# Optimization experiments

Measured on AMD Instinct MI355X. Metric: run time of the kernel, lower is better.

## Reference

```python
import jax, jax.numpy as jnp
import numpy as np

B, T, C, H, L, V = 64, 256, 256, 8, 6, 96
EPS = 1e-5


def _layernorm(x, w, b):
    m = x.mean(-1, keepdims=True)
    v = x.var(-1, keepdims=True)
    return (x - m) / jnp.sqrt(v + EPS) * w + b


def setup_inputs() -> dict:
    key = jax.random.key(0)
    ks = jax.random.split(key, 16)
    s = 0.05
    n = lambda k, sh: jax.random.normal(k, sh, jnp.float32) * s
    return {
        'idx': jax.random.randint(ks[0], (B, T), 0, V),
        'target': jax.random.randint(ks[1], (B, T), 0, V),
        'tok_emb': n(ks[2], (V, C)),
        'pos_emb': n(ks[3], (T, C)),
        'Wq': n(ks[4], (L, C, C)),
        'Wk': n(ks[5], (L, C, C)),
        'Wv': n(ks[6], (L, C, C)),
        'Wo': n(ks[7], (L, C, C)),
        'bo': jnp.zeros((L, C), jnp.float32),
        'W1': n(ks[8], (L, C, C)),
        'b1': jnp.zeros((L, C), jnp.float32),
        'W2': n(ks[9], (L, C, C)),
        'b2': jnp.zeros((L, C), jnp.float32),
        'ln1_w': jnp.ones((L, C), jnp.float32),
        'ln1_b': jnp.zeros((L, C), jnp.float32),
        'ln2_w': jnp.ones((L, C), jnp.float32),
        'ln2_b': jnp.zeros((L, C), jnp.float32),
        'lnf_w': jnp.ones((C,), jnp.float32),
        'lnf_b': jnp.zeros((C,), jnp.float32),
        'Wlm': n(ks[10], (C, V)),
        'blm': jnp.zeros((V,), jnp.float32),
    }


def _forward(idx, target, tok_emb, pos_emb, Wq, Wk, Wv, Wo, bo, W1, b1, W2, b2,
             ln1_w, ln1_b, ln2_w, ln2_b, lnf_w, lnf_b, Wlm, blm):
    Bc, Tc = idx.shape
    hs = C // H
    scale = C ** (-0.5)  # NOTE: original scales by n_embed**-0.5, not head_size**-0.5
    x = tok_emb[idx] + pos_emb[:Tc]              # [B,T,C]
    causal = jnp.tril(jnp.ones((Tc, Tc), bool))  # [T,T]
    for l in range(L):
        q = (x @ Wq[l]).reshape(Bc, Tc, H, hs)
        k = (x @ Wk[l]).reshape(Bc, Tc, H, hs)
        v = (x @ Wv[l]).reshape(Bc, Tc, H, hs)
        w = jnp.einsum('bqhd,bkhd->bhqk', q, k) * scale
        w = jnp.where(causal, w, -jnp.inf)
        w = jax.nn.softmax(w, axis=-1)
        att = jnp.einsum('bhqk,bkhd->bqhd', w, v).reshape(Bc, Tc, C)
        x = _layernorm(x + att @ Wo[l] + bo[l], ln1_w[l], ln1_b[l])  # post-residual LN
        h = jax.nn.relu(x @ W1[l] + b1[l]) @ W2[l] + b2[l]
        x = _layernorm(x + h, ln2_w[l], ln2_b[l])
    x = _layernorm(x, lnf_w, lnf_b)
    logits = (x @ Wlm + blm).reshape(Bc * Tc, V)
    logp = jax.nn.log_softmax(logits, axis=-1)
    nll = -jnp.take_along_axis(logp, target.reshape(-1, 1), axis=1)
    loss = nll.mean()
    return logits, loss


def reference(idx, target, tok_emb, pos_emb, Wq, Wk, Wv, Wo, bo, W1, b1, W2, b2,
              ln1_w, ln1_b, ln2_w, ln2_b, lnf_w, lnf_b, Wlm, blm):
    return _forward(idx, target, tok_emb, pos_emb, Wq, Wk, Wv, Wo, bo, W1, b1, W2, b2,
                    ln1_w, ln1_b, ln2_w, ln2_b, lnf_w, lnf_b, Wlm, blm)
```

## Files before the change

### kernel.cpp

```cpp
#include <hip/hip_runtime.h>

typedef unsigned short u16;

#define NT   16384
#define CDIM 256
#define LAYERS 6

using bf16x8 = __attribute__((ext_vector_type(8))) __bf16;
using f32x4  = __attribute__((ext_vector_type(4))) float;

__device__ __forceinline__ u16 f2bf(float x){
  unsigned u = __float_as_uint(x);
  u += 0x7fffu + ((u >> 16) & 1u);
  return (u16)(u >> 16);
}

__device__ __forceinline__ void gll16(const u16* g, u16* l){
  __builtin_amdgcn_global_load_lds(
      (const __attribute__((address_space(1))) unsigned int*)g,
      (__attribute__((address_space(3))) unsigned int*)l, 16, 0, 0);
}

__global__ __launch_bounds__(256) void wconv_k(
    const float* __restrict__ Wq, const float* __restrict__ Wk,
    const float* __restrict__ Wv, const float* __restrict__ Wo,
    const float* __restrict__ W1, const float* __restrict__ W2,
    const float* __restrict__ Wlm, u16* __restrict__ WT)
{
  __shared__ float tile[64][65];
  const int z = blockIdx.z;
  const float* src; u16* dst; int N = 256, Npad = 256;
  if (z < 18){
    const int l = z / 3, which = z % 3;
    const float* a[3] = {Wq, Wk, Wv};
    src = a[which] + (size_t)l * 65536;
    dst = WT + (size_t)l * 196608 + (size_t)which * 65536;
  } else if (z < 36){
    const int i = z - 18, j = i / 6, l = i % 6;
    const float* a[3] = {Wo, W1, W2};
    src = a[j] + (size_t)l * 65536;
    dst = WT + 1179648 + (size_t)(j * 6 + l) * 65536;
  } else {
    src = Wlm; dst = WT + 2359296; N = 96; Npad = 128;
  }
  const int n0 = blockIdx.y * 64, k0 = blockIdx.x * 64;
  if (n0 >= Npad) return;
  const int c = threadIdx.x & 63, r0 = threadIdx.x >> 6;
  #pragma unroll
  for (int i = 0; i < 16; ++i){
    const int r = r0 + i * 4;
    tile[r][c] = (n0 + c < N) ? src[(size_t)(k0 + r) * N + n0 + c] : 0.f;
  }
  __syncthreads();
  #pragma unroll
  for (int i = 0; i < 16; ++i){
    const int cp = r0 + i * 4;
    dst[(size_t)(n0 + cp) * CDIM + k0 + c] = f2bf(tile[c][cp]);
  }
}

__global__ __launch_bounds__(256) void embed_k(
    const int* __restrict__ idx, const float* __restrict__ tok,
    const float* __restrict__ pos, float* __restrict__ X, u16* __restrict__ Xb)
{
  const int w = threadIdx.x >> 6, l = threadIdx.x & 63;
  const int r = blockIdx.x * 4 + w;
  const int id = idx[r];
  float4 tv = *reinterpret_cast<const float4*>(tok + (size_t)id * CDIM + l * 4);
  float4 pv = *reinterpret_cast<const float4*>(pos + (size_t)(r & 255) * CDIM + l * 4);
  float4 y = {tv.x + pv.x, tv.y + pv.y, tv.z + pv.z, tv.w + pv.w};
  *reinterpret_cast<float4*>(X + (size_t)r * CDIM + l * 4) = y;
  union { u16 u[4]; uint2 q; } p;
  p.u[0] = f2bf(y.x); p.u[1] = f2bf(y.y); p.u[2] = f2bf(y.z); p.u[3] = f2bf(y.w);
  *reinterpret_cast<uint2*>(Xb + (size_t)r * CDIM + l * 4) = p.q;
}

template<int TM, int TN, int WR, int WC, bool DBUF,
         bool BIAS, bool RELU, bool RES, bool LN, bool OBF>
__global__ __launch_bounds__(256) void gemm_k(
    const u16* __restrict__ A, const u16* __restrict__ WT,
    const float* __restrict__ bias, const float* __restrict__ res,
    void* __restrict__ outp, u16* __restrict__ out2,
    const float* __restrict__ lnw, const float* __restrict__ lnb,
    int N, int ldo)
{
  constexpr int NB = DBUF ? 2 : 1;
  constexpr int MR = TM / WR / 16, NR = TN / WC / 16;
  __shared__ u16 As[NB * TM * 64];
  __shared__ u16 Bs[NB * TN * 64];
  const int t = threadIdx.x, l = t & 63, w = t >> 6;
  const int wr = w / WC, wc = w % WC;
  const int m0 = blockIdx.x * TM, n0 = blockIdx.y * TN;
  const int lr = l & 15, lk = (l >> 4) * 8;
  const int srow = t >> 3, sc8 = (t & 7) * 8;
  const int rb = wr * (TM / WR), cb = wc * (TN / WC);
  f32x4 acc[MR][NR] = {};

  auto stage = [&](int buf, int kt){
    const int k0 = kt * 64;
    u16* as = As + buf * (TM * 64);
    u16* bs = Bs + buf * (TN * 64);
    #pragma unroll
    for (int i = 0; i < TM / 32; ++i)
      gll16(A + (size_t)(m0 + srow + 32 * i) * CDIM + k0 + sc8, as + i * 2048 + t * 8);
    #pragma unroll
    for (int i = 0; i < TN / 32; ++i)
      gll16(WT + (size_t)(n0 + srow + 32 * i) * CDIM + k0 + sc8, bs + i * 2048 + t * 8);
  };
  auto compute = [&](int buf){
    const u16* as = As + buf * (TM * 64);
    const u16* bs = Bs + buf * (TN * 64);
    #pragma unroll
    for (int kk = 0; kk < 64; kk += 32){
      bf16x8 af[MR], bf[NR];
      #pragma unroll
      for (int m = 0; m < MR; ++m)
        af[m] = *reinterpret_cast<const bf16x8*>(&as[(rb + m * 16 + lr) * 64 + kk + lk]);
      #pragma unroll
      for (int n = 0; n < NR; ++n)
        bf[n] = *reinterpret_cast<const bf16x8*>(&bs[(cb + n * 16 + lr) * 64 + kk + lk]);
      #pragma unroll
      for (int m = 0; m < MR; ++m)
        #pragma unroll
        for (int n = 0; n < NR; ++n)
          acc[m][n] = __builtin_amdgcn_mfma_f32_16x16x32_bf16(af[m], bf[n], acc[m][n], 0, 0, 0);
    }
  };

  if constexpr (DBUF){
    stage(0, 0);
    __syncthreads();
    #pragma unroll
    for (int kt = 0; kt < 4; ++kt){
      if (kt < 3) stage((kt + 1) & 1, kt + 1);
      compute(kt & 1);
      if (kt < 3) __syncthreads();
    }
  } else {
    #pragma unroll
    for (int kt = 0; kt < 4; ++kt){
      if (kt) __syncthreads();
      stage(0, kt);
      __syncthreads();
      compute(0);
    }
  }

  const int rj = (l >> 4) * 4;
  if constexpr (LN){
    __shared__ float redS[TM][WC + 1], redQ[TM][WC + 1];
    #pragma unroll
    for (int m = 0; m < MR; ++m){
      #pragma unroll
      for (int j = 0; j < 4; ++j){
        const int lrow = rb + m * 16 + rj + j;
        const int grow = m0 + lrow;
        float s = 0.f, q = 0.f;
        #pragma unroll
        for (int n = 0; n < NR; ++n){
          const int gcol = cb + n * 16 + lr;
          float v = acc[m][n][j] + bias[gcol] + res[(size_t)grow * CDIM + gcol];
          acc[m][n][j] = v;
          s += v; q += v * v;
        }
        #pragma unroll
        for (int o = 1; o < 16; o <<= 1){ s += __shfl_xor(s, o); q += __shfl_xor(q, o); }
        if (lr == 0){ redS[lrow][wc] = s; redQ[lrow][wc] = q; }
      }
    }
    __syncthreads();
    #pragma unroll
    for (int m = 0; m < MR; ++m){
      #pragma unroll
      for (int j = 0; j < 4; ++j){
        const int lrow = rb + m * 16 + rj + j;
        const int grow = m0 + lrow;
        float s = 0.f, q = 0.f;
        #pragma unroll
        for (int c = 0; c < WC; ++c){ s += redS[lrow][c]; q += redQ[lrow][c]; }
        const float mean = s * (1.f / 256.f);
        const float rstd = rsqrtf(q * (1.f / 256.f) - mean * mean + 1e-5f);
        #pragma unroll
        for (int n = 0; n < NR; ++n){
          const int gcol = cb + n * 16 + lr;
          const size_t o = (size_t)grow * CDIM + gcol;
          const float y = (acc[m][n][j] - mean) * rstd * lnw[gcol] + lnb[gcol];
          ((float*)outp)[o] = y;
          out2[o] = f2bf(y);
        }
      }
    }
  } else {
    #pragma unroll
    for (int m = 0; m < MR; ++m){
      #pragma unroll
      for (int n = 0; n < NR; ++n){
        const int gcol = n0 + cb + n * 16 + lr;
        if (gcol < N){
          #pragma unroll
          for (int j = 0; j < 4; ++j){
            const int grow = m0 + rb + m * 16 + rj + j;
            const size_t o = (size_t)grow * ldo + gcol;
            float v = acc[m][n][j];
            if (BIAS) v += bias[gcol];
            if (RES)  v += res[o];
            if (RELU) v = fmaxf(v, 0.f);
            if (OBF) ((u16*)outp)[o] = f2bf(v);
            else     ((float*)outp)[o] = v;
          }
        }
      }
    }
  }
}

__global__ __launch_bounds__(256) void attn_k(
    const u16* __restrict__ QKV, u16* __restrict__ O)
{
  __shared__ u16 Vt[32][264];
  __shared__ u16 Ps[64][264];
  const int bh = blockIdx.x, b = bh >> 3, h = bh & 7;
  const size_t rbase = (size_t)b * 256 * 768;
  const int qc = h * 32, kc = 256 + h * 32, vc = 512 + h * 32;
  const int t = threadIdx.x, l = t & 63, w = t >> 6;
  const int lr = l & 15, lk = (l >> 4) * 8;

  {
    const uint4* vp = reinterpret_cast<const uint4*>(QKV + rbase + (size_t)t * 768 + vc);
    #pragma unroll
    for (int i = 0; i < 4; ++i){
      union { uint4 q; u16 u[8]; } p; p.q = vp[i];
      #pragma unroll
      for (int j = 0; j < 8; ++j) Vt[i * 8 + j][t] = p.u[j];
    }
  }
  bf16x8 kf[16];
  #pragma unroll
  for (int n = 0; n < 16; ++n)
    kf[n] = *reinterpret_cast<const bf16x8*>(QKV + rbase + (size_t)(n * 16 + lr) * 768 + kc + lk);
  __syncthreads();

  for (int c = 0; c < 4; ++c){
    const int rowb = c * 64 + w * 16;
    bf16x8 qa = *reinterpret_cast<const bf16x8*>(QKV + rbase + (size_t)(rowb + lr) * 768 + qc + lk);

    f32x4 s[16];
    #pragma unroll
    for (int n = 0; n < 16; ++n){
      f32x4 z = {};
      s[n] = __builtin_amdgcn_mfma_f32_16x16x32_bf16(qa, kf[n], z, 0, 0, 0);
    }

    float inv[4];
    const int prow = w * 16 + (l >> 4) * 4;
    #pragma unroll
    for (int j = 0; j < 4; ++j){
      const int qrow = rowb + (l >> 4) * 4 + j;
      float sv[16]; float mx = -1e30f;
      #pragma unroll
      for (int n = 0; n < 16; ++n){
        float vv = s[n][j] * 0.0625f;
        sv[n] = ((n * 16 + lr) <= qrow) ? vv : -1e30f;
        mx = fmaxf(mx, sv[n]);
      }
      #pragma unroll
      for (int o = 1; o < 16; o <<= 1) mx = fmaxf(mx, __shfl_xor(mx, o));
      float sum = 0.f;
      #pragma unroll
      for (int n = 0; n < 16; ++n){
        float p = __expf(sv[n] - mx);
        sum += p;
        Ps[prow + j][n * 16 + lr] = f2bf(p);
      }
      #pragma unroll
      for (int o = 1; o < 16; o <<= 1) sum += __shfl_xor(sum, o);
      inv[j] = 1.f / sum;
    }
    __syncthreads();

    f32x4 o0 = {}, o1 = {};
    #pragma unroll
    for (int kc2 = 0; kc2 < 8; ++kc2){
      bf16x8 pa = *reinterpret_cast<const bf16x8*>(&Ps[w * 16 + lr][kc2 * 32 + lk]);
      bf16x8 v0 = *reinterpret_cast<const bf16x8*>(&Vt[lr][kc2 * 32 + lk]);
      bf16x8 v1 = *reinterpret_cast<const bf16x8*>(&Vt[16 + lr][kc2 * 32 + lk]);
      o0 = __builtin_amdgcn_mfma_f32_16x16x32_bf16(pa, v0, o0, 0, 0, 0);
      o1 = __builtin_amdgcn_mfma_f32_16x16x32_bf16(pa, v1, o1, 0, 0, 0);
    }
    #pragma unroll
    for (int j = 0; j < 4; ++j){
      const int qrow = rowb + (l >> 4) * 4 + j;
      u16* op = O + (size_t)(b * 256 + qrow) * CDIM + h * 32;
      op[lr]      = f2bf(o0[j] * inv[j]);
      op[16 + lr] = f2bf(o1[j] * inv[j]);
    }
    __syncthreads();
  }
}

__global__ __launch_bounds__(256) void ln_k(
    const float* __restrict__ in, const float* __restrict__ w,
    const float* __restrict__ b, u16* __restrict__ Xb)
{
  const int wv = threadIdx.x >> 6, l = threadIdx.x & 63;
  const int r = blockIdx.x * 4 + wv;
  float4 v = *reinterpret_cast<const float4*>(in + (size_t)r * CDIM + l * 4);
  float s = v.x + v.y + v.z + v.w;
  float q = v.x * v.x + v.y * v.y + v.z * v.z + v.w * v.w;
  #pragma unroll
  for (int o = 32; o; o >>= 1){ s += __shfl_xor(s, o); q += __shfl_xor(q, o); }
  const float mean = s * (1.f / 256.f);
  const float var  = q * (1.f / 256.f) - mean * mean;
  const float rstd = rsqrtf(var + 1e-5f);
  float4 w4 = *reinterpret_cast<const float4*>(w + l * 4);
  float4 b4 = *reinterpret_cast<const float4*>(b + l * 4);
  union { u16 u[4]; uint2 q2; } p;
  p.u[0] = f2bf((v.x - mean) * rstd * w4.x + b4.x);
  p.u[1] = f2bf((v.y - mean) * rstd * w4.y + b4.y);
  p.u[2] = f2bf((v.z - mean) * rstd * w4.z + b4.z);
  p.u[3] = f2bf((v.w - mean) * rstd * w4.w + b4.w);
  *reinterpret_cast<uint2*>(Xb + (size_t)r * CDIM + l * 4) = p.q2;
}

__global__ __launch_bounds__(256) void nll_k(
    const float* __restrict__ logits, const int* __restrict__ target,
    float* __restrict__ nll)
{
  const int w = threadIdx.x >> 6, l = threadIdx.x & 63;
  const int r = blockIdx.x * 4 + w;
  const float* row = logits + (size_t)r * 96;
  float v0 = row[l];
  float v1 = (l < 32) ? row[64 + l] : -1e30f;
  float m = fmaxf(v0, v1);
  #pragma unroll
  for (int o = 32; o; o >>= 1) m = fmaxf(m, __shfl_xor(m, o));
  float s = __expf(v0 - m) + ((l < 32) ? __expf(v1 - m) : 0.f);
  #pragma unroll
  for (int o = 32; o; o >>= 1) s += __shfl_xor(s, o);
  if (l == 0) nll[r] = logf(s) + m - row[target[r]];
}

__global__ __launch_bounds__(256) void loss_k(
    const float* __restrict__ nll, float* __restrict__ out)
{
  __shared__ float rs[4];
  float s = 0.f;
  for (int i = threadIdx.x; i < NT; i += 256) s += nll[i];
  #pragma unroll
  for (int o = 32; o; o >>= 1) s += __shfl_xor(s, o);
  if ((threadIdx.x & 63) == 0) rs[threadIdx.x >> 6] = s;
  __syncthreads();
  if (threadIdx.x == 0) out[0] = (rs[0] + rs[1] + rs[2] + rs[3]) * (1.f / 16384.f);
}

extern "C" void kernel_launch(void* const* d_in, const int* in_sizes, int n_in,
                              void* d_out, int out_size, void* d_ws, size_t ws_size,
                              hipStream_t stream)
{
  const int*   idx    = (const int*)  d_in[0];
  const int*   target = (const int*)  d_in[1];
  const float* tok    = (const float*)d_in[2];
  const float* pos    = (const float*)d_in[3];
  const float* Wq     = (const float*)d_in[4];
  const float* Wk     = (const float*)d_in[5];
  const float* Wv     = (const float*)d_in[6];
  const float* Wo     = (const float*)d_in[7];
  const float* bo     = (const float*)d_in[8];
  const float* W1     = (const float*)d_in[9];
  const float* b1     = (const float*)d_in[10];
  const float* W2     = (const float*)d_in[11];
  const float* b2     = (const float*)d_in[12];
  const float* ln1w   = (const float*)d_in[13];
  const float* ln1b   = (const float*)d_in[14];
  const float* ln2w   = (const float*)d_in[15];
  const float* ln2b   = (const float*)d_in[16];
  const float* lnfw   = (const float*)d_in[17];
  const float* lnfb   = (const float*)d_in[18];
  const float* blm    = (const float*)d_in[20];
  float* out = (float*)d_out;

  char* ws = (char*)d_ws;
  float* X   = (float*)(ws);
  u16*   Xb  = (u16*)  (ws + (16u << 20));
  u16*   QKV = (u16*)  (ws + (24u << 20));
  u16*   O   = (u16*)  (ws + (48u << 20));
  u16*   hB  = (u16*)  (ws + (56u << 20));
  u16*   WT  = (u16*)  (ws + (64u << 20));
  float* nl  = (float*)(ws + (72u << 20));

  wconv_k<<<dim3(4, 4, 37), 256, 0, stream>>>(Wq, Wk, Wv, Wo, W1, W2,
                                              (const float*)d_in[19], WT);
  embed_k<<<NT / 4, 256, 0, stream>>>(idx, tok, pos, X, Xb);

  for (int l = 0; l < LAYERS; ++l){
    const u16* wqkv = WT + (size_t)l * 196608;
    const u16* wo   = WT + 1179648 + (size_t)(0 * 6 + l) * 65536;
    const u16* w1   = WT + 1179648 + (size_t)(1 * 6 + l) * 65536;
    const u16* w2   = WT + 1179648 + (size_t)(2 * 6 + l) * 65536;

    gemm_k<128, 128, 2, 2, false, false, false, false, false, true>
        <<<dim3(128, 6), 256, 0, stream>>>(
        Xb, wqkv, nullptr, nullptr, QKV, nullptr, nullptr, nullptr, 768, 768);
    attn_k<<<512, 256, 0, stream>>>(QKV, O);
    gemm_k<64, 256, 1, 4, true, true, false, true, true, false>
        <<<dim3(256, 1), 256, 0, stream>>>(
        O, wo, bo + l * 256, X, X, Xb, ln1w + l * 256, ln1b + l * 256, 256, 256);
    gemm_k<64, 256, 1, 4, true, true, true, false, false, true>
        <<<dim3(256, 1), 256, 0, stream>>>(
        Xb, w1, b1 + l * 256, nullptr, hB, nullptr, nullptr, nullptr, 256, 256);
    gemm_k<64, 256, 1, 4, true, true, false, true, true, false>
        <<<dim3(256, 1), 256, 0, stream>>>(
        hB, w2, b2 + l * 256, X, X, Xb, ln2w + l * 256, ln2b + l * 256, 256, 256);
  }

  ln_k<<<NT / 4, 256, 0, stream>>>(X, lnfw, lnfb, Xb);
  gemm_k<64, 128, 2, 2, true, true, false, false, false, false>
      <<<dim3(256, 1), 256, 0, stream>>>(
      Xb, WT + 2359296, blm, nullptr, out, nullptr, nullptr, nullptr, 96, 96);
  nll_k<<<NT / 4, 256, 0, stream>>>(out, target, nl);
  loss_k<<<1, 256, 0, stream>>>(nl, out + (size_t)NT * 96);
}
```

Measured before the change: 667.9 us.

## Keep residual stream in bf16 and restructure GEMM to stage full-K A tile

The fp32 residual copy X is dropped, so the residual stream is kept only in bf16 and the embed, LN-fused GEMM epilogues and final layernorm read and write bf16. The GEMM kernel is rewritten to load the whole 256-wide A tile into LDS in one pass and read weight fragments straight from global memory instead of double-buffered LDS staging. Blocks grow to 512 threads (8 waves). This cuts residual-stream traffic and per-k-step barriers, but adds bf16 rounding to the residual path and relies on cache hits for the global weight loads.

Result: slower. 684.3 us (+2.5%).

```diff
diff --git a/kernel.cpp b/kernel.cpp
--- a/kernel.cpp
+++ b/kernel.cpp
@@ -13,6 +13,9 @@
   unsigned u = __float_as_uint(x);
   u += 0x7fffu + ((u >> 16) & 1u);
   return (u16)(u >> 16);
+}
+__device__ __forceinline__ float bf2f(u16 u){
+  return __uint_as_float(((unsigned)u) << 16);
 }
 
 __device__ __forceinline__ void gll16(const u16* g, u16* l){
@@ -61,89 +64,57 @@
 
 __global__ __launch_bounds__(256) void embed_k(
     const int* __restrict__ idx, const float* __restrict__ tok,
-    const float* __restrict__ pos, float* __restrict__ X, u16* __restrict__ Xb)
+    const float* __restrict__ pos, u16* __restrict__ X)
 {
   const int w = threadIdx.x >> 6, l = threadIdx.x & 63;
   const int r = blockIdx.x * 4 + w;
   const int id = idx[r];
   float4 tv = *reinterpret_cast<const float4*>(tok + (size_t)id * CDIM + l * 4);
   float4 pv = *reinterpret_cast<const float4*>(pos + (size_t)(r & 255) * CDIM + l * 4);
-  float4 y = {tv.x + pv.x, tv.y + pv.y, tv.z + pv.z, tv.w + pv.w};
-  *reinterpret_cast<float4*>(X + (size_t)r * CDIM + l * 4) = y;
   union { u16 u[4]; uint2 q; } p;
-  p.u[0] = f2bf(y.x); p.u[1] = f2bf(y.y); p.u[2] = f2bf(y.z); p.u[3] = f2bf(y.w);
-  *reinterpret_cast<uint2*>(Xb + (size_t)r * CDIM + l * 4) = p.q;
-}
-
-template<int TM, int TN, int WR, int WC, bool DBUF,
-         bool BIAS, bool RELU, bool RES, bool LN, bool OBF>
-__global__ __launch_bounds__(256) void gemm_k(
+  p.u[0] = f2bf(tv.x + pv.x); p.u[1] = f2bf(tv.y + pv.y);
+  p.u[2] = f2bf(tv.z + pv.z); p.u[3] = f2bf(tv.w + pv.w);
+  *reinterpret_cast<uint2*>(X + (size_t)r * CDIM + l * 4) = p.q;
+}
+
+template<int TM, int TN, int WR, int WC, bool BIAS, bool RELU, bool RES, bool LN, bool F32OUT>
+__global__ __launch_bounds__(WR * WC * 64) void gemm2_k(
     const u16* __restrict__ A, const u16* __restrict__ WT,
-    const float* __restrict__ bias, const float* __restrict__ res,
-    void* __restrict__ outp, u16* __restrict__ out2,
-    const float* __restrict__ lnw, const float* __restrict__ lnb,
-    int N, int ldo)
-{
-  constexpr int NB = DBUF ? 2 : 1;
-  constexpr int MR = TM / WR / 16, NR = TN / WC / 16;
-  __shared__ u16 As[NB * TM * 64];
-  __shared__ u16 Bs[NB * TN * 64];
+    const float* __restrict__ bias, const u16* __restrict__ res,
+    void* __restrict__ outp, const float* __restrict__ lnw,
+    const float* __restrict__ lnb, int N, int ldo)
+{
+  constexpr int THREADS = WR * WC * 64;
+  constexpr int MR = TM / (WR * 16), NR = TN / (WC * 16);
+  __shared__ u16 As[TM * 256];
   const int t = threadIdx.x, l = t & 63, w = t >> 6;
   const int wr = w / WC, wc = w % WC;
   const int m0 = blockIdx.x * TM, n0 = blockIdx.y * TN;
   const int lr = l & 15, lk = (l >> 4) * 8;
-  const int srow = t >> 3, sc8 = (t & 7) * 8;
   const int rb = wr * (TM / WR), cb = wc * (TN / WC);
   f32x4 acc[MR][NR] = {};
 
-  auto stage = [&](int buf, int kt){
-    const int k0 = kt * 64;
-    u16* as = As + buf * (TM * 64);
-    u16* bs = Bs + buf * (TN * 64);
-    #pragma unroll
-    for (int i = 0; i < TM / 32; ++i)
-      gll16(A + (size_t)(m0 + srow + 32 * i) * CDIM + k0 + sc8, as + i * 2048 + t * 8);
-    #pragma unroll
-    for (int i = 0; i < TN / 32; ++i)
-      gll16(WT + (size_t)(n0 + srow + 32 * i) * CDIM + k0 + sc8, bs + i * 2048 + t * 8);
-  };
-  auto compute = [&](int buf){
-    const u16* as = As + buf * (TM * 64);
-    const u16* bs = Bs + buf * (TN * 64);
-    #pragma unroll
-    for (int kk = 0; kk < 64; kk += 32){
-      bf16x8 af[MR], bf[NR];
-      #pragma unroll
-      for (int m = 0; m < MR; ++m)
-        af[m] = *reinterpret_cast<const bf16x8*>(&as[(rb + m * 16 + lr) * 64 + kk + lk]);
+  #pragma unroll
+  for (int i = 0; i < TM * 32 / THREADS; ++i){
+    const int eo = (i * THREADS + t) * 8;
+    gll16(A + (size_t)(m0 + (eo >> 8)) * 256 + (eo & 255), As + eo);
+  }
+  __syncthreads();
+
+  #pragma unroll
+  for (int kk = 0; kk < 256; kk += 32){
+    bf16x8 af[MR], bf[NR];
+    #pragma unroll
+    for (int m = 0; m < MR; ++m)
+      af[m] = *reinterpret_cast<const bf16x8*>(&As[(rb + m * 16 + lr) * 256 + kk + lk]);
+    #pragma unroll
+    for (int n = 0; n < NR; ++n)
+      bf[n] = *reinterpret_cast<const bf16x8*>(WT + (size_t)(n0 + cb + n * 16 + lr) * 256 + kk + lk);
+    #pragma unroll
+    for (int m = 0; m < MR; ++m)
       #pragma unroll
       for (int n = 0; n < NR; ++n)
-        bf[n] = *reinterpret_cast<const bf16x8*>(&bs[(cb + n * 16 + lr) * 64 + kk + lk]);
-      #pragma unroll
-      for (int m = 0; m < MR; ++m)
-        #pragma unroll
-        for (int n = 0; n < NR; ++n)
-          acc[m][n] = __builtin_amdgcn_mfma_f32_16x16x32_bf16(af[m], bf[n], acc[m][n], 0, 0, 0);
-    }
-  };
-
-  if constexpr (DBUF){
-    stage(0, 0);
-    __syncthreads();
-    #pragma unroll
-    for (int kt = 0; kt < 4; ++kt){
-      if (kt < 3) stage((kt + 1) & 1, kt + 1);
-      compute(kt & 1);
-      if (kt < 3) __syncthreads();
-    }
-  } else {
-    #pragma unroll
-    for (int kt = 0; kt < 4; ++kt){
-      if (kt) __syncthreads();
-      stage(0, kt);
-      __syncthreads();
-      compute(0);
-    }
+        acc[m][n] = __builtin_amdgcn_mfma_f32_16x16x32_bf16(af[m], bf[n], acc[m][n], 0, 0, 0);
   }
 
   const int rj = (l >> 4) * 4;
@@ -159,7 +130,7 @@
         #pragma unroll
         for (int n = 0; n < NR; ++n){
           const int gcol = cb + n * 16 + lr;
-          float v = acc[m][n][j] + bias[gcol] + res[(size_t)grow * CDIM + gcol];
+          float v = acc[m][n][j] + bias[gcol] + bf2f(res[(size_t)grow * CDIM + gcol]);
           acc[m][n][j] = v;
           s += v; q += v * v;
         }
@@ -183,10 +154,8 @@
         #pragma unroll
         for (int n = 0; n < NR; ++n){
           const int gcol = cb + n * 16 + lr;
-          const size_t o = (size_t)grow * CDIM + gcol;
           const float y = (acc[m][n][j] - mean) * rstd * lnw[gcol] + lnb[gcol];
-          ((float*)outp)[o] = y;
-          out2[o] = f2bf(y);
+          ((u16*)outp)[(size_t)grow * CDIM + gcol] = f2bf(y);
         }
       }
     }
@@ -203,10 +172,10 @@
             const size_t o = (size_t)grow * ldo + gcol;
             float v = acc[m][n][j];
             if (BIAS) v += bias[gcol];
-            if (RES)  v += res[o];
+            if (RES)  v += bf2f(res[o]);
             if (RELU) v = fmaxf(v, 0.f);
-            if (OBF) ((u16*)outp)[o] = f2bf(v);
-            else     ((float*)outp)[o] = v;
+            if (F32OUT) ((float*)outp)[o] = v;
+            else        ((u16*)outp)[o] = f2bf(v);
           }
         }
       }
@@ -298,28 +267,29 @@
   }
 }
 
-__global__ __launch_bounds__(256) void ln_k(
-    const float* __restrict__ in, const float* __restrict__ w,
-    const float* __restrict__ b, u16* __restrict__ Xb)
+__global__ __launch_bounds__(256) void lnf_k(
+    const u16* __restrict__ in, const float* __restrict__ w,
+    const float* __restrict__ b, u16* __restrict__ out)
 {
   const int wv = threadIdx.x >> 6, l = threadIdx.x & 63;
   const int r = blockIdx.x * 4 + wv;
-  float4 v = *reinterpret_cast<const float4*>(in + (size_t)r * CDIM + l * 4);
-  float s = v.x + v.y + v.z + v.w;
-  float q = v.x * v.x + v.y * v.y + v.z * v.z + v.w * v.w;
+  union { uint2 q; u16 u[4]; } iv;
+  iv.q = *reinterpret_cast<const uint2*>(in + (size_t)r * CDIM + l * 4);
+  float v0 = bf2f(iv.u[0]), v1 = bf2f(iv.u[1]), v2 = bf2f(iv.u[2]), v3 = bf2f(iv.u[3]);
+  float s = v0 + v1 + v2 + v3;
+  float q = v0 * v0 + v1 * v1 + v2 * v2 + v3 * v3;
   #pragma unroll
   for (int o = 32; o; o >>= 1){ s += __shfl_xor(s, o); q += __shfl_xor(q, o); }
   const float mean = s * (1.f / 256.f);
-  const float var  = q * (1.f / 256.f) - mean * mean;
-  const float rstd = rsqrtf(var + 1e-5f);
+  const float rstd = rsqrtf(q * (1.f / 256.f) - mean * mean + 1e-5f);
   float4 w4 = *reinterpret_cast<const float4*>(w + l * 4);
   float4 b4 = *reinterpret_cast<const float4*>(b + l * 4);
   union { u16 u[4]; uint2 q2; } p;
-  p.u[0] = f2bf((v.x - mean) * rstd * w4.x + b4.x);
-  p.u[1] = f2bf((v.y - mean) * rstd * w4.y + b4.y);
-  p.u[2] = f2bf((v.z - mean) * rstd * w4.z + b4.z);
-  p.u[3] = f2bf((v.w - mean) * rstd * w4.w + b4.w);
-  *reinterpret_cast<uint2*>(Xb + (size_t)r * CDIM + l * 4) = p.q2;
+  p.u[0] = f2bf((v0 - mean) * rstd * w4.x + b4.x);
+  p.u[1] = f2bf((v1 - mean) * rstd * w4.y + b4.y);
+  p.u[2] = f2bf((v2 - mean) * rstd * w4.z + b4.z);
+  p.u[3] = f2bf((v3 - mean) * rstd * w4.w + b4.w);
+  *reinterpret_cast<uint2*>(out + (size_t)r * CDIM + l * 4) = p.q2;
 }
 
 __global__ __launch_bounds__(256) void nll_k(
@@ -380,17 +350,17 @@
   float* out = (float*)d_out;
 
   char* ws = (char*)d_ws;
-  float* X   = (float*)(ws);
-  u16*   Xb  = (u16*)  (ws + (16u << 20));
-  u16*   QKV = (u16*)  (ws + (24u << 20));
-  u16*   O   = (u16*)  (ws + (48u << 20));
-  u16*   hB  = (u16*)  (ws + (56u << 20));
-  u16*   WT  = (u16*)  (ws + (64u << 20));
-  float* nl  = (float*)(ws + (72u << 20));
+  u16*   X   = (u16*)  (ws);
+  u16*   QKV = (u16*)  (ws + ( 8u << 20));
+  u16*   O   = (u16*)  (ws + (32u << 20));
+  u16*   hB  = (u16*)  (ws + (40u << 20));
+  u16*   Xf  = (u16*)  (ws + (48u << 20));
+  u16*   WT  = (u16*)  (ws + (56u << 20));
+  float* nl  = (float*)(ws + (64u << 20));
 
   wconv_k<<<dim3(4, 4, 37), 256, 0, stream>>>(Wq, Wk, Wv, Wo, W1, W2,
                                               (const float*)d_in[19], WT);
-  embed_k<<<NT / 4, 256, 0, stream>>>(idx, tok, pos, X, Xb);
+  embed_k<<<NT / 4, 256, 0, stream>>>(idx, tok, pos, X);
 
   for (int l = 0; l < LAYERS; ++l){
     const u16* wqkv = WT + (size_t)l * 196608;
@@ -398,25 +368,25 @@
     const u16* w1   = WT + 1179648 + (size_t)(1 * 6 + l) * 65536;
     const u16* w2   = WT + 1179648 + (size_t)(2 * 6 + l) * 65536;
 
-    gemm_k<128, 128, 2, 2, false, false, false, false, false, true>
-        <<<dim3(128, 6), 256, 0, stream>>>(
-        Xb, wqkv, nullptr, nullptr, QKV, nullptr, nullptr, nullptr, 768, 768);
+    gemm2_k<128, 128, 2, 4, false, false, false, false, false>
+        <<<dim3(128, 6), 512, 0, stream>>>(
+        X, wqkv, nullptr, nullptr, QKV, nullptr, nullptr, 768, 768);
     attn_k<<<512, 256, 0, stream>>>(QKV, O);
-    gemm_k<64, 256, 1, 4, true, true, false, true, true, false>
-        <<<dim3(256, 1), 256, 0, stream>>>(
-        O, wo, bo + l * 256, X, X, Xb, ln1w + l * 256, ln1b + l * 256, 256, 256);
-    gemm_k<64, 256, 1, 4, true, true, true, false, false, true>
-        <<<dim3(256, 1), 256, 0, stream>>>(
-        Xb, w1, b1 + l * 256, nullptr, hB, nullptr, nullptr, nullptr, 256, 256);
-    gemm_k<64, 256, 1, 4, true, true, false, true, true, false>
-        <<<dim3(256, 1), 256, 0, stream>>>(
-        hB, w2, b2 + l * 256, X, X, Xb, ln2w + l * 256, ln2b + l * 256, 256, 256);
-  }
-
-  ln_k<<<NT / 4, 256, 0, stream>>>(X, lnfw, lnfb, Xb);
-  gemm_k<64, 128, 2, 2, true, true, false, false, false, false>
-      <<<dim3(256, 1), 256, 0, stream>>>(
-      Xb, WT + 2359296, blm, nullptr, out, nullptr, nullptr, nullptr, 96, 96);
+    gemm2_k<64, 256, 2, 4, true, false, true, true, false>
+        <<<dim3(256, 1), 512, 0, stream>>>(
+        O, wo, bo + l * 256, X, X, ln1w + l * 256, ln1b + l * 256, 256, 256);
+    gemm2_k<64, 128, 2, 4, true, true, false, false, false>
+        <<<dim3(256, 2), 512, 0, stream>>>(
+        X, w1, b1 + l * 256, nullptr, hB, nullptr, nullptr, 256, 256);
+    gemm2_k<64, 256, 2, 4, true, false, true, true, false>
+        <<<dim3(256, 1), 512, 0, stream>>>(
+        hB, w2, b2 + l * 256, X, X, ln2w + l * 256, ln2b + l * 256, 256, 256);
+  }
+
+  lnf_k<<<NT / 4, 256, 0, stream>>>(X, lnfw, lnfb, Xf);
+  gemm2_k<64, 128, 2, 4, true, false, false, false, true>
+      <<<dim3(256, 1), 512, 0, stream>>>(
+      Xf, WT + 2359296, blm, nullptr, out, nullptr, nullptr, 96, 96);
   nll_k<<<NT / 4, 256, 0, stream>>>(out, target, nl);
   loss_k<<<1, 256, 0, stream>>>(nl, out + (size_t)NT * 96);
 }
```
